# Optimization experiments

Measured on AMD Instinct MI355X. Metric: run time of the kernel, lower is better.

Reference implementation:

```python
import jax, jax.numpy as jnp
import numpy as np

SIGMA = 0.5          # cone height of the distance field
B, NV, NF, MAXC = 32, 6890, 13776, 8
NC = NF * MAXC       # padded number of collision pair slots


def setup_inputs() -> dict:
    key = jax.random.key(0)
    ks = jax.random.split(key, 8)
    return {
        "pose": jax.random.normal(ks[0], (B, 72), jnp.float32),
        "joints": jax.random.normal(ks[1], (B, 24, 3), jnp.float32),
        "points": jax.random.normal(ks[2], (B, 118, 3), jnp.float32),
        "keypoints": jax.random.normal(ks[3], (B, 118, 3), jnp.float32),
        "vertices": jax.random.normal(ks[4], (B, NV, 3), jnp.float32),
        "weight": jnp.ones((1,), jnp.float32),
        "faces": jax.random.randint(ks[5], (NF, 3), 0, NV, dtype=jnp.int32),
        "collision_idxs": jax.random.randint(ks[6], (B, NC, 2), 0, NF, dtype=jnp.int32),
    }


def _cone_point2plane(cone_tris, query_tris):
    """Conic distance-field penetration (point2plane), vectorized over pairs.
    cone_tris/query_tris: [B, C, 3 verts, 3 xyz]. Returns [B, C]."""
    c = cone_tris.mean(axis=-2)                              # centroid [B,C,3]
    e1 = cone_tris[..., 1, :] - cone_tris[..., 0, :]
    e2 = cone_tris[..., 2, :] - cone_tris[..., 0, :]
    n = jnp.cross(e1, e2)
    n = n / (jnp.linalg.norm(n, axis=-1, keepdims=True) + 1e-8)
    d = query_tris - c[..., None, :]                         # [B,C,3,3]
    h = jnp.einsum('bcvk,bck->bcv', d, n)                    # signed plane dist
    r = jnp.linalg.norm(d, axis=-1)                          # dist to centroid
    phi = jnp.maximum(SIGMA - r, 0.0)                        # linear cone field
    pen = jnp.where(h < 0, phi * h * h, 0.0)                 # penetrating verts only
    return pen.sum(axis=-1)


def reference(pose, joints, points, keypoints, vertices, weight, faces, collision_idxs):
    # polygons = verts.view(-1,3)[faces_idx]  ->  per-batch face gather
    tris = jnp.take(vertices, faces, axis=1)                 # [B,NF,3,3]
    recv_idx = collision_idxs[..., 0]
    intr_idx = collision_idxs[..., 1]
    valid = recv_idx >= 0                                    # -1 padding slots

    def gather(idx):
        idx = jnp.maximum(idx, 0)[:, :, None, None]
        return jnp.take_along_axis(tris, idx, axis=1)        # [B,NC,3,3]

    recv = gather(recv_idx)
    intr = gather(intr_idx)
    # symmetric penetration: intruder verts in receiver's field and vice versa
    pen = _cone_point2plane(recv, intr) + _cone_point2plane(intr, recv)
    loss = jnp.where(valid, pen, 0.0).sum() / B
    return loss * weight[0]
```

## Files before the change

kernel.cpp:

```cpp
#include <hip/hip_runtime.h>

#define SIGMA 0.5f
#define BB 32
#define NVV 6890
#define NFF 13776
#define MAXC 8
#define NCC (NFF * MAXC)

#define REC_HALFS 16
#define REC_BYTES ((size_t)BB * NFF * REC_HALFS * sizeof(_Float16))

#define PAIRS_PER_BLOCK 1024
#define SLOTS4 ((NCC + PAIRS_PER_BLOCK - 1) / PAIRS_PER_BLOCK)
#define NPART (BB * SLOTS4)

typedef int v4i __attribute__((ext_vector_type(4)));

union RecU {
    uint4    u[2];
    _Float16 h[16];
};

__device__ __forceinline__ float3 loadv3(const float* __restrict__ p) {
    return make_float3(p[0], p[1], p[2]);
}

__global__ __launch_bounds__(256) void face_kernel(
    const float* __restrict__ vertices,
    const int*   __restrict__ faces,
    uint4*       __restrict__ rec)
{
    const int i = blockIdx.x * blockDim.x + threadIdx.x;
    if (i >= BB * NFF) return;
    const int b = i / NFF;
    const int f = i - b * NFF;

    const float* vb = vertices + (size_t)b * (NVV * 3);
    const int i0 = faces[f * 3 + 0];
    const int i1 = faces[f * 3 + 1];
    const int i2 = faces[f * 3 + 2];
    float3 v0 = loadv3(vb + (size_t)i0 * 3);
    float3 v1 = loadv3(vb + (size_t)i1 * 3);
    float3 v2 = loadv3(vb + (size_t)i2 * 3);

    const float third = 1.0f / 3.0f;
    float cx = (v0.x + v1.x + v2.x) * third;
    float cy = (v0.y + v1.y + v2.y) * third;
    float cz = (v0.z + v1.z + v2.z) * third;

    float e1x = v1.x - v0.x, e1y = v1.y - v0.y, e1z = v1.z - v0.z;
    float e2x = v2.x - v0.x, e2y = v2.y - v0.y, e2z = v2.z - v0.z;
    float nx = e1y * e2z - e1z * e2y;
    float ny = e1z * e2x - e1x * e2z;
    float nz = e1x * e2y - e1y * e2x;
    float inv = 1.0f / (sqrtf(nx * nx + ny * ny + nz * nz) + 1e-8f);
    nx *= inv; ny *= inv; nz *= inv;

    RecU r;
    r.h[0]  = (_Float16)cx;   r.h[1]  = (_Float16)cy;   r.h[2]  = (_Float16)cz;
    r.h[3]  = (_Float16)nx;   r.h[4]  = (_Float16)ny;   r.h[5]  = (_Float16)nz;
    r.h[6]  = (_Float16)v0.x; r.h[7]  = (_Float16)v0.y; r.h[8]  = (_Float16)v0.z;
    r.h[9]  = (_Float16)v1.x; r.h[10] = (_Float16)v1.y; r.h[11] = (_Float16)v1.z;
    r.h[12] = (_Float16)v2.x; r.h[13] = (_Float16)v2.y; r.h[14] = (_Float16)v2.z;
    r.h[15] = (_Float16)0.0f;

    uint4* dst = rec + (size_t)i * 2;
    dst[0] = r.u[0];
    dst[1] = r.u[1];
}

__device__ __forceinline__ float penSide(const RecU& C, const RecU& Q) {
    float cx = (float)C.h[0], cy = (float)C.h[1], cz = (float)C.h[2];
    float nx = (float)C.h[3], ny = (float)C.h[4], nz = (float)C.h[5];
    float pen = 0.0f;
#pragma unroll
    for (int v = 0; v < 3; ++v) {
        float dx = (float)Q.h[6 + 3 * v + 0] - cx;
        float dy = (float)Q.h[6 + 3 * v + 1] - cy;
        float dz = (float)Q.h[6 + 3 * v + 2] - cz;
        float h = dx * nx + dy * ny + dz * nz;
        float r = sqrtf(dx * dx + dy * dy + dz * dz);
        float phi = fmaxf(SIGMA - r, 0.0f);
        pen += (h < 0.0f) ? phi * h * h : 0.0f;
    }
    return pen;
}

__global__ __launch_bounds__(256) void pair_kernel(
    const uint4* __restrict__ rec,
    const int*   __restrict__ cidx,
    float*       __restrict__ partials)
{
    const int b    = blockIdx.x;
    const int slot = blockIdx.y;
    const int base = slot * PAIRS_PER_BLOCK + threadIdx.x * 4;
    float pen = 0.0f;

    if (base < NCC) {
        const v4i* c4 = (const v4i*)(cidx + (size_t)b * NCC * 2)
                        + ((size_t)slot * 512 + threadIdx.x * 2);
        v4i pr0 = __builtin_nontemporal_load(c4);
        v4i pr1 = __builtin_nontemporal_load(c4 + 1);

        int fi[8] = { pr0.x, pr0.y, pr0.z, pr0.w, pr1.x, pr1.y, pr1.z, pr1.w };
        bool valid[4];
#pragma unroll
        for (int p = 0; p < 4; ++p) valid[p] = fi[2 * p] >= 0;
#pragma unroll
        for (int k = 0; k < 8; ++k) fi[k] = fi[k] < 0 ? 0 : fi[k];

        RecU R[8];
        const uint4* rbase = rec + (size_t)b * NFF * 2;
#pragma unroll
        for (int k = 0; k < 8; ++k) {
            const uint4* rp = rbase + (size_t)fi[k] * 2;
            R[k].u[0] = rp[0];
            R[k].u[1] = rp[1];
        }

#pragma unroll
        for (int p = 0; p < 4; ++p) {
            float pp = penSide(R[2 * p], R[2 * p + 1])
                     + penSide(R[2 * p + 1], R[2 * p]);
            pen += valid[p] ? pp : 0.0f;
        }
    }

#pragma unroll
    for (int off = 32; off > 0; off >>= 1)
        pen += __shfl_down(pen, off, 64);

    __shared__ float smem[4];
    const int lane = threadIdx.x & 63;
    const int wv   = threadIdx.x >> 6;
    if (lane == 0) smem[wv] = pen;
    __syncthreads();
    if (threadIdx.x == 0)
        partials[(size_t)b * SLOTS4 + slot] = smem[0] + smem[1] + smem[2] + smem[3];
}

__global__ __launch_bounds__(1024) void reduce_kernel(
    const float* __restrict__ partials,
    const float* __restrict__ weight,
    float*       __restrict__ out)
{
    float s = 0.0f;
    for (int i = threadIdx.x; i < NPART; i += 1024)
        s += partials[i];
#pragma unroll
    for (int off = 32; off > 0; off >>= 1)
        s += __shfl_down(s, off, 64);

    __shared__ float smem[16];
    const int lane = threadIdx.x & 63;
    const int wv   = threadIdx.x >> 6;
    if (lane == 0) smem[wv] = s;
    __syncthreads();
    if (threadIdx.x == 0) {
        float t = 0.0f;
#pragma unroll
        for (int w = 0; w < 16; ++w) t += smem[w];
        out[0] = t * weight[0] * (1.0f / (float)BB);
    }
}

__global__ void init_kernel(float* __restrict__ accum) { accum[0] = 0.0f; }

__device__ __forceinline__ float conePen(float3 a0, float3 a1, float3 a2,
                                         float3 q0, float3 q1, float3 q2) {
    const float third = 1.0f / 3.0f;
    float cx = (a0.x + a1.x + a2.x) * third;
    float cy = (a0.y + a1.y + a2.y) * third;
    float cz = (a0.z + a1.z + a2.z) * third;
    float e1x = a1.x - a0.x, e1y = a1.y - a0.y, e1z = a1.z - a0.z;
    float e2x = a2.x - a0.x, e2y = a2.y - a0.y, e2z = a2.z - a0.z;
    float nx = e1y * e2z - e1z * e2y;
    float ny = e1z * e2x - e1x * e2z;
    float nz = e1x * e2y - e1y * e2x;
    float inv = 1.0f / (sqrtf(nx * nx + ny * ny + nz * nz) + 1e-8f);
    nx *= inv; ny *= inv; nz *= inv;
    float3 q[3] = {q0, q1, q2};
    float pen = 0.0f;
#pragma unroll
    for (int v = 0; v < 3; ++v) {
        float dx = q[v].x - cx, dy = q[v].y - cy, dz = q[v].z - cz;
        float h = dx * nx + dy * ny + dz * nz;
        float r = sqrtf(dx * dx + dy * dy + dz * dz);
        float phi = fmaxf(SIGMA - r, 0.0f);
        pen += (h < 0.0f) ? phi * h * h : 0.0f;
    }
    return pen;
}

__global__ __launch_bounds__(256) void pen_direct(
    const float* __restrict__ vertices, const int* __restrict__ faces,
    const int2* __restrict__ cidx, float* __restrict__ accum)
{
    const int i = blockIdx.x * blockDim.x + threadIdx.x;
    float pen = 0.0f;
    if (i < BB * NCC) {
        const int b = i / NCC;
        const int2 pr = cidx[i];
        if (pr.x >= 0) {
            const int f0 = pr.x;
            const int f1 = pr.y < 0 ? 0 : pr.y;
            const float* vb = vertices + (size_t)b * (NVV * 3);
            float3 a0 = loadv3(vb + (size_t)faces[f0*3+0] * 3);
            float3 a1 = loadv3(vb + (size_t)faces[f0*3+1] * 3);
            float3 a2 = loadv3(vb + (size_t)faces[f0*3+2] * 3);
            float3 b0 = loadv3(vb + (size_t)faces[f1*3+0] * 3);
            float3 b1 = loadv3(vb + (size_t)faces[f1*3+1] * 3);
            float3 b2 = loadv3(vb + (size_t)faces[f1*3+2] * 3);
            pen = conePen(a0,a1,a2,b0,b1,b2) + conePen(b0,b1,b2,a0,a1,a2);
        }
    }
#pragma unroll
    for (int off = 32; off > 0; off >>= 1)
        pen += __shfl_down(pen, off, 64);
    __shared__ float smem[4];
    const int lane = threadIdx.x & 63;
    const int wv   = threadIdx.x >> 6;
    if (lane == 0) smem[wv] = pen;
    __syncthreads();
    if (threadIdx.x == 0)
        atomicAdd(accum, smem[0] + smem[1] + smem[2] + smem[3]);
}

__global__ void fin_kernel(const float* __restrict__ accum,
                           const float* __restrict__ weight,
                           float* __restrict__ out)
{
    out[0] = accum[0] * weight[0] * (1.0f / (float)BB);
}

extern "C" void kernel_launch(void* const* d_in, const int* in_sizes, int n_in,
                              void* d_out, int out_size, void* d_ws, size_t ws_size,
                              hipStream_t stream) {
    const float* vertices = (const float*)d_in[4];
    const float* weight   = (const float*)d_in[5];
    const int*   faces    = (const int*)d_in[6];
    const int*   cidx     = (const int*)d_in[7];
    float* out = (float*)d_out;

    if (ws_size >= REC_BYTES + NPART * sizeof(float) + 256) {
        uint4* rec      = (uint4*)d_ws;
        float* partials = (float*)((char*)d_ws + REC_BYTES);

        const int totalFaces = BB * NFF;
        face_kernel<<<dim3((totalFaces + 255) / 256), dim3(256), 0, stream>>>(
            vertices, faces, rec);
        pair_kernel<<<dim3(BB, SLOTS4), dim3(256), 0, stream>>>(rec, cidx, partials);
        reduce_kernel<<<dim3(1), dim3(1024), 0, stream>>>(partials, weight, out);
    } else {
        float* accum = (float*)d_ws;
        const int totalPairs = BB * NCC;
        init_kernel<<<dim3(1), dim3(1), 0, stream>>>(accum);
        pen_direct<<<dim3((totalPairs + 255) / 256), dim3(256), 0, stream>>>(
            vertices, faces, (const int2*)cidx, accum);
        fin_kernel<<<dim3(1), dim3(1), 0, stream>>>(accum, weight, out);
    }
}
```

Measured before the change: 138.8 us.

## Stage per-batch vertices in LDS for face records and halve pairs per thread

The face kernel now launches one block per (batch, face-chunk). Each block loads that batch's whole vertex array into shared memory as fp16, then gathers triangle vertices from LDS instead of doing scattered global loads. This means every block reloads the full vertex array (24 chunks per batch). Separately, the pair kernel processes 2 pairs per thread instead of 4, doubling the block count to raise parallelism and reduce registers, but it also doubles the partials the reduce kernel must sum.

```diff
diff --git a/kernel.cpp b/kernel.cpp
--- a/kernel.cpp
+++ b/kernel.cpp
@@ -10,9 +10,12 @@
 #define REC_HALFS 16
 #define REC_BYTES ((size_t)BB * NFF * REC_HALFS * sizeof(_Float16))
 
-#define PAIRS_PER_BLOCK 1024
-#define SLOTS4 ((NCC + PAIRS_PER_BLOCK - 1) / PAIRS_PER_BLOCK)
-#define NPART (BB * SLOTS4)
+#define PAIRS_PER_BLOCK 512
+#define SLOTS2 ((NCC + PAIRS_PER_BLOCK - 1) / PAIRS_PER_BLOCK)
+#define NPART (BB * SLOTS2)
+
+#define FSPLIT 24
+#define FPB (NFF / FSPLIT)
 
 typedef int v4i __attribute__((ext_vector_type(4)));
 
@@ -25,48 +28,64 @@
     return make_float3(p[0], p[1], p[2]);
 }
 
-__global__ __launch_bounds__(256) void face_kernel(
+__global__ __launch_bounds__(256) void face_lds_kernel(
     const float* __restrict__ vertices,
     const int*   __restrict__ faces,
     uint4*       __restrict__ rec)
 {
-    const int i = blockIdx.x * blockDim.x + threadIdx.x;
-    if (i >= BB * NFF) return;
-    const int b = i / NFF;
-    const int f = i - b * NFF;
-
-    const float* vb = vertices + (size_t)b * (NVV * 3);
-    const int i0 = faces[f * 3 + 0];
-    const int i1 = faces[f * 3 + 1];
-    const int i2 = faces[f * 3 + 2];
-    float3 v0 = loadv3(vb + (size_t)i0 * 3);
-    float3 v1 = loadv3(vb + (size_t)i1 * 3);
-    float3 v2 = loadv3(vb + (size_t)i2 * 3);
-
-    const float third = 1.0f / 3.0f;
-    float cx = (v0.x + v1.x + v2.x) * third;
-    float cy = (v0.y + v1.y + v2.y) * third;
-    float cz = (v0.z + v1.z + v2.z) * third;
-
-    float e1x = v1.x - v0.x, e1y = v1.y - v0.y, e1z = v1.z - v0.z;
-    float e2x = v2.x - v0.x, e2y = v2.y - v0.y, e2z = v2.z - v0.z;
-    float nx = e1y * e2z - e1z * e2y;
-    float ny = e1z * e2x - e1x * e2z;
-    float nz = e1x * e2y - e1y * e2x;
-    float inv = 1.0f / (sqrtf(nx * nx + ny * ny + nz * nz) + 1e-8f);
-    nx *= inv; ny *= inv; nz *= inv;
-
-    RecU r;
-    r.h[0]  = (_Float16)cx;   r.h[1]  = (_Float16)cy;   r.h[2]  = (_Float16)cz;
-    r.h[3]  = (_Float16)nx;   r.h[4]  = (_Float16)ny;   r.h[5]  = (_Float16)nz;
-    r.h[6]  = (_Float16)v0.x; r.h[7]  = (_Float16)v0.y; r.h[8]  = (_Float16)v0.z;
-    r.h[9]  = (_Float16)v1.x; r.h[10] = (_Float16)v1.y; r.h[11] = (_Float16)v1.z;
-    r.h[12] = (_Float16)v2.x; r.h[13] = (_Float16)v2.y; r.h[14] = (_Float16)v2.z;
-    r.h[15] = (_Float16)0.0f;
-
-    uint4* dst = rec + (size_t)i * 2;
-    dst[0] = r.u[0];
-    dst[1] = r.u[1];
+    __shared__ _Float16 sv[NVV * 3];
+
+    const int b  = blockIdx.x;
+    const int s  = blockIdx.y;
+    const int t  = threadIdx.x;
+
+    const float2* vb2 = (const float2*)(vertices + (size_t)b * (NVV * 3));
+    uint* svu = (uint*)sv;
+    for (int j = t; j < (NVV * 3) / 2; j += 256) {
+        float2 v = vb2[j];
+        union { uint u; _Float16 h[2]; } pk;
+        pk.h[0] = (_Float16)v.x;
+        pk.h[1] = (_Float16)v.y;
+        svu[j] = pk.u;
+    }
+    __syncthreads();
+
+    const int f0 = s * FPB;
+    for (int r = t; r < FPB; r += 256) {
+        const int f = f0 + r;
+        const int i0 = faces[f * 3 + 0];
+        const int i1 = faces[f * 3 + 1];
+        const int i2 = faces[f * 3 + 2];
+
+        float v0x = (float)sv[i0*3+0], v0y = (float)sv[i0*3+1], v0z = (float)sv[i0*3+2];
+        float v1x = (float)sv[i1*3+0], v1y = (float)sv[i1*3+1], v1z = (float)sv[i1*3+2];
+        float v2x = (float)sv[i2*3+0], v2y = (float)sv[i2*3+1], v2z = (float)sv[i2*3+2];
+
+        const float third = 1.0f / 3.0f;
+        float cx = (v0x + v1x + v2x) * third;
+        float cy = (v0y + v1y + v2y) * third;
+        float cz = (v0z + v1z + v2z) * third;
+
+        float e1x = v1x - v0x, e1y = v1y - v0y, e1z = v1z - v0z;
+        float e2x = v2x - v0x, e2y = v2y - v0y, e2z = v2z - v0z;
+        float nx = e1y * e2z - e1z * e2y;
+        float ny = e1z * e2x - e1x * e2z;
+        float nz = e1x * e2y - e1y * e2x;
+        float inv = 1.0f / (sqrtf(nx * nx + ny * ny + nz * nz) + 1e-8f);
+        nx *= inv; ny *= inv; nz *= inv;
+
+        RecU rc;
+        rc.h[0]  = (_Float16)cx;  rc.h[1]  = (_Float16)cy;  rc.h[2]  = (_Float16)cz;
+        rc.h[3]  = (_Float16)nx;  rc.h[4]  = (_Float16)ny;  rc.h[5]  = (_Float16)nz;
+        rc.h[6]  = (_Float16)v0x; rc.h[7]  = (_Float16)v0y; rc.h[8]  = (_Float16)v0z;
+        rc.h[9]  = (_Float16)v1x; rc.h[10] = (_Float16)v1y; rc.h[11] = (_Float16)v1z;
+        rc.h[12] = (_Float16)v2x; rc.h[13] = (_Float16)v2y; rc.h[14] = (_Float16)v2z;
+        rc.h[15] = (_Float16)0.0f;
+
+        uint4* dst = rec + ((size_t)b * NFF + f) * 2;
+        dst[0] = rc.u[0];
+        dst[1] = rc.u[1];
+    }
 }
 
 __device__ __forceinline__ float penSide(const RecU& C, const RecU& Q) {
@@ -93,37 +112,31 @@
 {
     const int b    = blockIdx.x;
     const int slot = blockIdx.y;
-    const int base = slot * PAIRS_PER_BLOCK + threadIdx.x * 4;
+    const int base = slot * PAIRS_PER_BLOCK + threadIdx.x * 2;
     float pen = 0.0f;
 
     if (base < NCC) {
         const v4i* c4 = (const v4i*)(cidx + (size_t)b * NCC * 2)
-                        + ((size_t)slot * 512 + threadIdx.x * 2);
-        v4i pr0 = __builtin_nontemporal_load(c4);
-        v4i pr1 = __builtin_nontemporal_load(c4 + 1);
-
-        int fi[8] = { pr0.x, pr0.y, pr0.z, pr0.w, pr1.x, pr1.y, pr1.z, pr1.w };
-        bool valid[4];
-#pragma unroll
-        for (int p = 0; p < 4; ++p) valid[p] = fi[2 * p] >= 0;
-#pragma unroll
-        for (int k = 0; k < 8; ++k) fi[k] = fi[k] < 0 ? 0 : fi[k];
-
-        RecU R[8];
+                        + ((size_t)slot * 256 + threadIdx.x);
+        v4i pr = __builtin_nontemporal_load(c4);
+
+        const bool valid0 = pr.x >= 0;
+        const bool valid1 = pr.z >= 0;
+        int fi[4] = { pr.x < 0 ? 0 : pr.x, pr.y < 0 ? 0 : pr.y,
+                      pr.z < 0 ? 0 : pr.z, pr.w < 0 ? 0 : pr.w };
+
+        RecU R[4];
         const uint4* rbase = rec + (size_t)b * NFF * 2;
 #pragma unroll
-        for (int k = 0; k < 8; ++k) {
+        for (int k = 0; k < 4; ++k) {
             const uint4* rp = rbase + (size_t)fi[k] * 2;
             R[k].u[0] = rp[0];
             R[k].u[1] = rp[1];
         }
 
-#pragma unroll
-        for (int p = 0; p < 4; ++p) {
-            float pp = penSide(R[2 * p], R[2 * p + 1])
-                     + penSide(R[2 * p + 1], R[2 * p]);
-            pen += valid[p] ? pp : 0.0f;
-        }
+        float p0 = penSide(R[0], R[1]) + penSide(R[1], R[0]);
+        float p1 = penSide(R[2], R[3]) + penSide(R[3], R[2]);
+        pen = (valid0 ? p0 : 0.0f) + (valid1 ? p1 : 0.0f);
     }
 
 #pragma unroll
@@ -136,7 +149,7 @@
     if (lane == 0) smem[wv] = pen;
     __syncthreads();
     if (threadIdx.x == 0)
-        partials[(size_t)b * SLOTS4 + slot] = smem[0] + smem[1] + smem[2] + smem[3];
+        partials[(size_t)b * SLOTS2 + slot] = smem[0] + smem[1] + smem[2] + smem[3];
 }
 
 __global__ __launch_bounds__(1024) void reduce_kernel(
@@ -246,10 +259,9 @@
         uint4* rec      = (uint4*)d_ws;
         float* partials = (float*)((char*)d_ws + REC_BYTES);
 
-        const int totalFaces = BB * NFF;
-        face_kernel<<<dim3((totalFaces + 255) / 256), dim3(256), 0, stream>>>(
+        face_lds_kernel<<<dim3(BB, FSPLIT), dim3(256), 0, stream>>>(
             vertices, faces, rec);
-        pair_kernel<<<dim3(BB, SLOTS4), dim3(256), 0, stream>>>(rec, cidx, partials);
+        pair_kernel<<<dim3(BB, SLOTS2), dim3(256), 0, stream>>>(rec, cidx, partials);
         reduce_kernel<<<dim3(1), dim3(1024), 0, stream>>>(partials, weight, out);
     } else {
         float* accum = (float*)d_ws;
```

New measurement: 143.1 us. +3.1%, slower.

## Process one collision pair per thread and skip gathers for invalid pairs

Applied to the files above, without the earlier changes.

The pair kernel now gives each thread a single collision pair instead of four, launching four times as many blocks. Record gathers are skipped entirely when the pair is padding, so invalid slots cost no memory traffic. Each wave writes its own partial directly, which removes the shared-memory block reduction and its barrier, and the final reduce reads the partials as float4. In exchange there is less memory-level parallelism per thread (two gathers in flight instead of eight), and the partials buffer is four times larger.

```diff
diff --git a/kernel.cpp b/kernel.cpp
--- a/kernel.cpp
+++ b/kernel.cpp
@@ -10,11 +10,10 @@
 #define REC_HALFS 16
 #define REC_BYTES ((size_t)BB * NFF * REC_HALFS * sizeof(_Float16))
 
-#define PAIRS_PER_BLOCK 1024
-#define SLOTS4 ((NCC + PAIRS_PER_BLOCK - 1) / PAIRS_PER_BLOCK)
-#define NPART (BB * SLOTS4)
-
-typedef int v4i __attribute__((ext_vector_type(4)));
+#define SLOTS1 ((NCC + 255) / 256)
+#define NPART (BB * SLOTS1 * 4)
+
+typedef int v2i __attribute__((ext_vector_type(2)));
 
 union RecU {
     uint4    u[2];
@@ -93,36 +92,20 @@
 {
     const int b    = blockIdx.x;
     const int slot = blockIdx.y;
-    const int base = slot * PAIRS_PER_BLOCK + threadIdx.x * 4;
-    float pen = 0.0f;
-
-    if (base < NCC) {
-        const v4i* c4 = (const v4i*)(cidx + (size_t)b * NCC * 2)
-                        + ((size_t)slot * 512 + threadIdx.x * 2);
-        v4i pr0 = __builtin_nontemporal_load(c4);
-        v4i pr1 = __builtin_nontemporal_load(c4 + 1);
-
-        int fi[8] = { pr0.x, pr0.y, pr0.z, pr0.w, pr1.x, pr1.y, pr1.z, pr1.w };
-        bool valid[4];
-#pragma unroll
-        for (int p = 0; p < 4; ++p) valid[p] = fi[2 * p] >= 0;
-#pragma unroll
-        for (int k = 0; k < 8; ++k) fi[k] = fi[k] < 0 ? 0 : fi[k];
-
-        RecU R[8];
-        const uint4* rbase = rec + (size_t)b * NFF * 2;
-#pragma unroll
-        for (int k = 0; k < 8; ++k) {
-            const uint4* rp = rbase + (size_t)fi[k] * 2;
-            R[k].u[0] = rp[0];
-            R[k].u[1] = rp[1];
-        }
-
-#pragma unroll
-        for (int p = 0; p < 4; ++p) {
-            float pp = penSide(R[2 * p], R[2 * p + 1])
-                     + penSide(R[2 * p + 1], R[2 * p]);
-            pen += valid[p] ? pp : 0.0f;
+    const int p    = slot * 256 + threadIdx.x;
+    float pen = 0.0f;
+
+    if (p < NCC) {
+        const v2i* c2 = (const v2i*)(cidx + (size_t)b * NCC * 2) + p;
+        v2i pr = __builtin_nontemporal_load(c2);
+        if (pr.x >= 0) {
+            const int f1 = pr.y < 0 ? 0 : pr.y;
+            const uint4* ra = rec + ((size_t)b * NFF + pr.x) * 2;
+            const uint4* rb = rec + ((size_t)b * NFF + f1) * 2;
+            RecU A, B;
+            A.u[0] = ra[0]; A.u[1] = ra[1];
+            B.u[0] = rb[0]; B.u[1] = rb[1];
+            pen = penSide(A, B) + penSide(B, A);
         }
     }
 
@@ -130,13 +113,10 @@
     for (int off = 32; off > 0; off >>= 1)
         pen += __shfl_down(pen, off, 64);
 
-    __shared__ float smem[4];
     const int lane = threadIdx.x & 63;
     const int wv   = threadIdx.x >> 6;
-    if (lane == 0) smem[wv] = pen;
-    __syncthreads();
-    if (threadIdx.x == 0)
-        partials[(size_t)b * SLOTS4 + slot] = smem[0] + smem[1] + smem[2] + smem[3];
+    if (lane == 0)
+        partials[(((size_t)b * SLOTS1 + slot) << 2) + wv] = pen;
 }
 
 __global__ __launch_bounds__(1024) void reduce_kernel(
@@ -144,9 +124,12 @@
     const float* __restrict__ weight,
     float*       __restrict__ out)
 {
+    const float4* p4 = (const float4*)partials;
     float s = 0.0f;
-    for (int i = threadIdx.x; i < NPART; i += 1024)
-        s += partials[i];
+    for (int i = threadIdx.x; i < NPART / 4; i += 1024) {
+        float4 v = p4[i];
+        s += (v.x + v.y) + (v.z + v.w);
+    }
 #pragma unroll
     for (int off = 32; off > 0; off >>= 1)
         s += __shfl_down(s, off, 64);
@@ -249,7 +232,8 @@
         const int totalFaces = BB * NFF;
         face_kernel<<<dim3((totalFaces + 255) / 256), dim3(256), 0, stream>>>(
             vertices, faces, rec);
-        pair_kernel<<<dim3(BB, SLOTS4), dim3(256), 0, stream>>>(rec, cidx, partials);
+        pair_kernel<<<dim3(BB, SLOTS1), dim3(256), 0, stream>>>(
+            rec, cidx, partials);
         reduce_kernel<<<dim3(1), dim3(1024), 0, stream>>>(partials, weight, out);
     } else {
         float* accum = (float*)d_ws;
```

Result: no change. 139.9 us (+0.8%).
